# Performance work log

Hardware: AMD Instinct MI355X
Metric: run time of the kernel (lower is better)

Reference implementation:

```python
import jax, jax.numpy as jnp
import numpy as np

N_EMBD = 1024
N_HEAD = 16
HEAD_DIM = N_EMBD // N_HEAD
B, T = 2, 2048


def setup_inputs() -> dict:
    key = jax.random.key(0)
    ks = jax.random.split(key, 12)
    s = 0.02
    inp = {
        "x": jax.random.normal(ks[0], (B, T, N_EMBD), dtype=jnp.float32),
        "ln1_g": jnp.ones((N_EMBD,), jnp.float32),
        "ln1_b": jnp.zeros((N_EMBD,), jnp.float32),
        "ln2_g": jnp.ones((N_EMBD,), jnp.float32),
        "ln2_b": jnp.zeros((N_EMBD,), jnp.float32),
        "W_qkv": jax.random.normal(ks[1], (N_EMBD, 3 * N_EMBD), jnp.float32) * s,
        "b_qkv": jnp.zeros((3 * N_EMBD,), jnp.float32),
        "W_o": jax.random.normal(ks[2], (N_EMBD, N_EMBD), jnp.float32) * s,
        "b_o": jnp.zeros((N_EMBD,), jnp.float32),
        "W_fc": jax.random.normal(ks[3], (N_EMBD, 4 * N_EMBD), jnp.float32) * s,
        "b_fc": jnp.zeros((4 * N_EMBD,), jnp.float32),
        "W_proj": jax.random.normal(ks[4], (4 * N_EMBD, N_EMBD), jnp.float32) * s,
        "b_proj": jnp.zeros((N_EMBD,), jnp.float32),
    }
    return inp


def _layernorm(x, g, b, eps=1e-5):
    mu = jnp.mean(x, axis=-1, keepdims=True)
    var = jnp.var(x, axis=-1, keepdims=True)
    return (x - mu) * jax.lax.rsqrt(var + eps) * g + b


def _block(x, ln1_g, ln1_b, ln2_g, ln2_b, W_qkv, b_qkv, W_o, b_o, W_fc, b_fc, W_proj, b_proj):
    # --- attention sub-block (pre-LN) ---
    h = _layernorm(x, ln1_g, ln1_b)
    qkv = h @ W_qkv + b_qkv                     # [B,T,3E]
    q, k, v = jnp.split(qkv, 3, axis=-1)
    def split_heads(t):
        return t.reshape(B, T, N_HEAD, HEAD_DIM).transpose(0, 2, 1, 3)  # [B,H,T,D]
    q, k, v = split_heads(q), split_heads(k), split_heads(v)
    scores = jnp.einsum("bhqd,bhkd->bhqk", q, k) / (HEAD_DIM ** 0.5)
    causal = jnp.tril(jnp.ones((T, T), dtype=bool))
    scores = jnp.where(causal, scores, jnp.float32(-jnp.inf))
    probs = jax.nn.softmax(scores, axis=-1)
    attn = jnp.einsum("bhqk,bhkd->bhqd", probs, v)        # [B,H,T,D]
    attn = attn.transpose(0, 2, 1, 3).reshape(B, T, N_EMBD)
    x = x + attn @ W_o + b_o
    # --- MLP sub-block (pre-LN) ---
    h = _layernorm(x, ln2_g, ln2_b)
    h = jax.nn.gelu(h @ W_fc + b_fc, approximate=False)
    x = x + h @ W_proj + b_proj
    return x


def reference(x, ln1_g, ln1_b, ln2_g, ln2_b, W_qkv, b_qkv, W_o, b_o, W_fc, b_fc, W_proj, b_proj):
    return _block(x, ln1_g, ln1_b, ln2_g, ln2_b, W_qkv, b_qkv, W_o, b_o, W_fc, b_fc, W_proj, b_proj)
```

## Files before the change

### kernel.cpp

```cpp
#include <hip/hip_runtime.h>
#include <hip/hip_bf16.h>


#define TT 2048
#define EE 1024
#define NH 16
#define HD 64

#define AS1 __attribute__((address_space(1)))
#define AS3 __attribute__((address_space(3)))

using bf16x8 = __bf16 __attribute__((ext_vector_type(8)));
using bf16x4 = __bf16 __attribute__((ext_vector_type(4)));
using f32x4  = float __attribute__((ext_vector_type(4)));

template<int N> __device__ __forceinline__ void vm_wait() {
    if constexpr (N == 0)      asm volatile("s_waitcnt vmcnt(0)" ::: "memory");
    else if constexpr (N == 2) asm volatile("s_waitcnt vmcnt(2)" ::: "memory");
    else if constexpr (N == 3) asm volatile("s_waitcnt vmcnt(3)" ::: "memory");
    else if constexpr (N == 4) asm volatile("s_waitcnt vmcnt(4)" ::: "memory");
    else if constexpr (N == 6) asm volatile("s_waitcnt vmcnt(6)" ::: "memory");
    else                       asm volatile("s_waitcnt vmcnt(8)" ::: "memory");
}

__device__ __forceinline__ float gelu_fast(float v) {
    float z  = v * 0.70710678118f;
    float az = fabsf(z);
    float t  = __builtin_amdgcn_rcpf(__builtin_fmaf(0.3275911f, az, 1.0f));
    float p  = t * __builtin_fmaf(t,
                   __builtin_fmaf(t,
                     __builtin_fmaf(t,
                       __builtin_fmaf(t, 1.061405429f, -1.453152027f),
                       1.421413741f),
                     -0.284496736f),
                   0.254829592f);
    float e  = __expf(-az * az);
    float er = copysignf(1.0f - p * e, z);
    return 0.5f * v * (1.0f + er);
}

__global__ __launch_bounds__(256) void convt_kernel(const float* __restrict__ W,
                                                    __bf16* __restrict__ WT,
                                                    int K, int N) {
    __shared__ __bf16 t[32][33];
    int n0 = blockIdx.x * 32, k0 = blockIdx.y * 32;
    int tid = threadIdx.x;
    int r = tid >> 3, c4 = (tid & 7) * 4;
    float4 v = *(const float4*)(W + (size_t)(k0 + r) * N + n0 + c4);
    t[r][c4 + 0] = (__bf16)v.x; t[r][c4 + 1] = (__bf16)v.y;
    t[r][c4 + 2] = (__bf16)v.z; t[r][c4 + 3] = (__bf16)v.w;
    __syncthreads();
    bf16x4 o;
    o[0] = t[c4 + 0][r]; o[1] = t[c4 + 1][r];
    o[2] = t[c4 + 2][r]; o[3] = t[c4 + 3][r];
    *(bf16x4*)(WT + (size_t)(n0 + r) * K + k0 + c4) = o;
}

__global__ __launch_bounds__(256) void ln_kernel(const float* __restrict__ x,
                                                 const float* __restrict__ g,
                                                 const float* __restrict__ bta,
                                                 __bf16* __restrict__ out) {
    int row = blockIdx.x;
    int tid = threadIdx.x;
    const float4 xv = *(const float4*)(x + (size_t)row * EE + tid * 4);
    float s  = xv.x + xv.y + xv.z + xv.w;
    float ss = xv.x*xv.x + xv.y*xv.y + xv.z*xv.z + xv.w*xv.w;
    __shared__ float rs[256], rss[256];
    rs[tid] = s; rss[tid] = ss;
    __syncthreads();
    for (int st = 128; st > 0; st >>= 1) {
        if (tid < st) { rs[tid] += rs[tid+st]; rss[tid] += rss[tid+st]; }
        __syncthreads();
    }
    float mean = rs[0] * (1.0f / EE);
    float var  = rss[0] * (1.0f / EE) - mean * mean;
    float rstd = rsqrtf(var + 1e-5f);
    const float4 gv = *(const float4*)(g + tid * 4);
    const float4 bv = *(const float4*)(bta + tid * 4);
    bf16x4 ov;
    ov[0] = (__bf16)((xv.x - mean) * rstd * gv.x + bv.x);
    ov[1] = (__bf16)((xv.y - mean) * rstd * gv.y + bv.y);
    ov[2] = (__bf16)((xv.z - mean) * rstd * gv.z + bv.z);
    ov[3] = (__bf16)((xv.w - mean) * rstd * gv.w + bv.w);
    *(bf16x4*)(out + (size_t)row * EE + tid * 4) = ov;
}

template<int TM, int TN, bool GELU, bool RESID, bool QKV, bool ATOMIC, typename CT>
__global__ __launch_bounds__(256) void gemm_bt_kernel(const __bf16* __restrict__ A,
                                                      const __bf16* __restrict__ BT,
                                                      const float* __restrict__ bias,
                                                      const float* resid, CT* C,
                                                      __bf16* vT,
                                                      int M, int N, int K) {
    constexpr int MT = TM / 32;
    constexpr int NT = TN / 32;
    constexpr int LOADS = TM / 64 + TN / 64;
    constexpr int NBUF  = ATOMIC ? 3 : ((LOADS <= 3) ? 4 : 3);
    constexpr int DEPTH = NBUF - 1;
    constexpr int WAITN = (DEPTH - 1) * LOADS;
    __shared__ __align__(16) __bf16 As[NBUF][TM][32];
    __shared__ __align__(16) __bf16 Bs[NBUF][TN][32];
    int tid = threadIdx.x, wave = tid >> 6, lane = tid & 63;
    int quad = lane >> 4, l16 = lane & 15;
    int wm = wave >> 1, wn = wave & 1;
    int m0 = blockIdx.y * TM, n0 = blockIdx.x * TN;

    const int klen = ATOMIC ? (K >> 1) : K;
    const int koff = ATOMIC ? (int)blockIdx.z * klen : 0;

    f32x4 acc[MT][NT] = {};

    int srow = wave * 16 + (lane >> 2);
    int scol = (((lane & 3) ^ ((lane >> 3) & 3)) * 8);
    int xcol = ((quad ^ ((l16 >> 1) & 3)) * 8);

    auto STAGE = [&](int buf, int kt) {
        int kb = koff + (kt << 5);
#pragma unroll
        for (int p = 0; p < TM / 64; p++) {
            const __bf16* g = A + (size_t)(m0 + p * 64 + srow) * K + kb + scol;
            __builtin_amdgcn_global_load_lds((AS1 const void*)g,
                                             (AS3 void*)&As[buf][p * 64 + wave * 16][0],
                                             16, 0, 0);
        }
#pragma unroll
        for (int p = 0; p < TN / 64; p++) {
            const __bf16* g = BT + (size_t)(n0 + p * 64 + srow) * K + kb + scol;
            __builtin_amdgcn_global_load_lds((AS1 const void*)g,
                                             (AS3 void*)&Bs[buf][p * 64 + wave * 16][0],
                                             16, 0, 0);
        }
    };

    auto COMPUTE = [&](int cur) {
        bf16x8 af[MT], bfr[NT];
#pragma unroll
        for (int mt = 0; mt < MT; mt++)
            af[mt] = *(const bf16x8*)(&As[cur][wm * (MT * 16) + mt * 16 + l16][xcol]);
#pragma unroll
        for (int nt = 0; nt < NT; nt++)
            bfr[nt] = *(const bf16x8*)(&Bs[cur][wn * (NT * 16) + nt * 16 + l16][xcol]);
#pragma unroll
        for (int mt = 0; mt < MT; mt++)
#pragma unroll
            for (int nt = 0; nt < NT; nt++)
                acc[mt][nt] = __builtin_amdgcn_mfma_f32_16x16x32_bf16(af[mt], bfr[nt],
                                                                      acc[mt][nt], 0, 0, 0);
    };

    const int nk = klen >> 5;
#pragma unroll
    for (int i = 0; i < DEPTH; ++i) STAGE(i, i);
    vm_wait<WAITN>();
    __builtin_amdgcn_s_barrier();

    int t = 0;
    for (; t + DEPTH < nk; ++t) {
        STAGE((t + DEPTH) % NBUF, t + DEPTH);
        COMPUTE(t % NBUF);
        vm_wait<WAITN>();
        __builtin_amdgcn_s_barrier();
    }
    for (; t < nk; ++t) {
        COMPUTE(t % NBUF);
        if (t + 1 < nk) {
            int rem = nk - 2 - t;
            if (rem >= 1) vm_wait<LOADS>();
            else          vm_wait<0>();
            __builtin_amdgcn_s_barrier();
        }
    }

#pragma unroll
    for (int nt = 0; nt < NT; nt++) {
        int c = n0 + wn * (NT * 16) + nt * 16 + l16;
        float bv = (!ATOMIC || blockIdx.z == 0) ? bias[c] : 0.0f;
#pragma unroll
        for (int mt = 0; mt < MT; mt++) {
#pragma unroll
            for (int r = 0; r < 4; r++) {
                int row = m0 + wm * (MT * 16) + mt * 16 + quad * 4 + r;
                float v = acc[mt][nt][r] + bv;
                if (GELU)  v = gelu_fast(v);
                if (RESID) v += resid[(size_t)row * N + c];
                if (ATOMIC) {
                    atomicAdd((float*)&C[(size_t)row * N + c], v);
                } else if (!QKV) {
                    C[(size_t)row * N + c] = (CT)v;
                } else {
                    if (c < 2 * EE) {
                        ((__bf16*)C)[(size_t)row * (2 * EE) + c] = (__bf16)v;
                    } else {
                        int cv = c - 2 * EE;
                        int bb = row >> 11, tt = row & (TT - 1);
                        vT[((size_t)(bb * NH + (cv >> 6)) * HD + (cv & 63)) * TT + tt] =
                            (__bf16)v;
                    }
                }
            }
        }
    }
}

__global__ __launch_bounds__(64) void flash_attn_kernel(const __bf16* __restrict__ qkv,
                                                        const __bf16* __restrict__ vT,
                                                        __bf16* __restrict__ out) {
    int h = blockIdx.y, b = blockIdx.z;
    int lane = threadIdx.x & 63;
    int quad = lane >> 4, l16 = lane & 15;

    __shared__ __align__(16) __bf16 Ps[16 * 136];

    size_t base = (size_t)b * TT * (2 * EE);
    int qt = (int)gridDim.x - 1 - (int)blockIdx.x;
    int q0 = qt * 16;

    const __bf16* kb2  = qkv + base + EE + h * HD;
    const __bf16* vrow = vT + (size_t)(b * NH + h) * HD * TT + (size_t)l16 * TT + quad * 8;

    const __bf16* qp = qkv + base + (size_t)(q0 + l16) * (2 * EE) + h * HD;
    bf16x8 aq0 = *(const bf16x8*)(qp + quad * 8);
    bf16x8 aq1 = *(const bf16x8*)(qp + 32 + quad * 8);

    f32x4 oacc[4] = {};
    float lsum[4] = {0.f, 0.f, 0.f, 0.f};
    int qg_base = q0 + quad * 4;
    int nIter = (qt >> 3) + 1;

    for (int kt = 0; kt < nIter; ++kt) {
        int k0 = kt * 128;

        bf16x8 bk0[8], bk1[8];
#pragma unroll
        for (int nt = 0; nt < 8; nt++) {
            const __bf16* kp = kb2 + (size_t)(k0 + nt * 16 + l16) * (2 * EE) + quad * 8;
            bk0[nt] = *(const bf16x8*)(kp);
            bk1[nt] = *(const bf16x8*)(kp + 32);
        }

        f32x4 s[8];
#pragma unroll
        for (int nt = 0; nt < 8; nt++) {
            f32x4 z = {};
            z = __builtin_amdgcn_mfma_f32_16x16x32_bf16(aq0, bk0[nt], z, 0, 0, 0);
            s[nt] = __builtin_amdgcn_mfma_f32_16x16x32_bf16(aq1, bk1[nt], z, 0, 0, 0);
        }

        bf16x8 vf[4][4];
#pragma unroll
        for (int dt = 0; dt < 4; dt++)
#pragma unroll
            for (int w = 0; w < 4; w++)
                vf[dt][w] = *(const bf16x8*)(vrow + (size_t)dt * (16 * TT) + k0 + w * 32);

        bool maskt = (kt == nIter - 1);
#pragma unroll
        for (int nt = 0; nt < 8; nt++) {
            int key = k0 + nt * 16 + l16;
            int cb = 2 * nt + (l16 >> 3);
#pragma unroll
            for (int r = 0; r < 4; r++) {
                float p;
                if (maskt && key > qg_base + r) p = 0.0f;
                else p = __expf(fminf(s[nt][r] * 0.125f, 30.0f));
                lsum[r] += p;
                int q = quad * 4 + r;
                int col = (((cb & 8) | ((cb - 2 * q) & 7)) << 3) | (l16 & 7);
                Ps[q * 136 + col] = (__bf16)p;
            }
        }

#pragma unroll
        for (int w = 0; w < 4; w++) {
            int cbr = 4 * w + quad;
            int colr = ((cbr & 8) | ((cbr - 2 * l16) & 7)) << 3;
            bf16x8 ap = *(const bf16x8*)(&Ps[l16 * 136 + colr]);
#pragma unroll
            for (int dt = 0; dt < 4; dt++)
                oacc[dt] = __builtin_amdgcn_mfma_f32_16x16x32_bf16(ap, vf[dt][w],
                                                                   oacc[dt], 0, 0, 0);
        }
    }

#pragma unroll
    for (int off = 1; off < 16; off <<= 1)
#pragma unroll
        for (int r = 0; r < 4; r++) lsum[r] += __shfl_xor(lsum[r], off);
#pragma unroll
    for (int dt = 0; dt < 4; dt++) {
#pragma unroll
        for (int r = 0; r < 4; r++) {
            int qg = qg_base + r;
            out[((size_t)b * TT + qg) * EE + h * HD + dt * 16 + l16] =
                (__bf16)(oacc[dt][r] / lsum[r]);
        }
    }
}

extern "C" void kernel_launch(void* const* d_in, const int* in_sizes, int n_in,
                              void* d_out, int out_size, void* d_ws, size_t ws_size,
                              hipStream_t stream) {
    const float* x     = (const float*)d_in[0];
    const float* ln1g  = (const float*)d_in[1];
    const float* ln1b  = (const float*)d_in[2];
    const float* ln2g  = (const float*)d_in[3];
    const float* ln2b  = (const float*)d_in[4];
    const float* Wqkv  = (const float*)d_in[5];
    const float* bqkv  = (const float*)d_in[6];
    const float* Wo    = (const float*)d_in[7];
    const float* bo    = (const float*)d_in[8];
    const float* Wfc   = (const float*)d_in[9];
    const float* bfc   = (const float*)d_in[10];
    const float* Wproj = (const float*)d_in[11];
    const float* bproj = (const float*)d_in[12];
    float* out = (float*)d_out;

    const int M = 2 * TT;

    __bf16* ws = (__bf16*)d_ws;
    __bf16* regQ   = ws;
    __bf16* regS   = ws + 16777216;
    __bf16* WfcT   = ws + 20971520;
    __bf16* qkv    = regQ;
    __bf16* vT     = regQ + 8388608;
    __bf16* WqkvT  = regQ + 12582912;
    __bf16* WoT    = regQ + 15728640;
    __bf16* ff     = regQ;
    __bf16* h1 = regS, *atn = regS, *h2 = regS;
    __bf16* WprojT = regS;
    float*  x1 = out;

    convt_kernel<<<dim3(3 * EE / 32, EE / 32), 256, 0, stream>>>(Wqkv, WqkvT, EE, 3 * EE);
    convt_kernel<<<dim3(EE / 32, EE / 32), 256, 0, stream>>>(Wo, WoT, EE, EE);
    convt_kernel<<<dim3(4 * EE / 32, EE / 32), 256, 0, stream>>>(Wfc, WfcT, EE, 4 * EE);

    ln_kernel<<<M, 256, 0, stream>>>(x, ln1g, ln1b, h1);
    gemm_bt_kernel<128, 128, false, false, true, false, __bf16>
        <<<dim3(3 * EE / 128, M / 128), 256, 0, stream>>>(
        h1, WqkvT, bqkv, nullptr, qkv, vT, M, 3 * EE, EE);
    flash_attn_kernel<<<dim3(TT / 16, NH, 2), 64, 0, stream>>>(qkv, vT, atn);
    gemm_bt_kernel<128, 64, false, true, false, false, float>
        <<<dim3(EE / 64, M / 128), 256, 0, stream>>>(
        atn, WoT, bo, x, x1, nullptr, M, EE, EE);
    ln_kernel<<<M, 256, 0, stream>>>(x1, ln2g, ln2b, h2);
    gemm_bt_kernel<128, 128, true, false, false, false, __bf16>
        <<<dim3(4 * EE / 128, M / 128), 256, 0, stream>>>(
        h2, WfcT, bfc, nullptr, ff, nullptr, M, 4 * EE, EE);
    convt_kernel<<<dim3(EE / 32, 4 * EE / 32), 256, 0, stream>>>(Wproj, WprojT, 4 * EE, EE);
    gemm_bt_kernel<128, 64, false, false, false, true, float>
        <<<dim3(EE / 64, M / 128, 2), 256, 0, stream>>>(
        ff, WprojT, bproj, nullptr, out, nullptr, M, EE, 4 * EE);
}
```

Measured before the change: 507.1 us.

## Share K tiles across two waves via LDS with register prefetch in flash attention

The attention kernel now runs two waves per block, each handling 16 query rows, so a block covers 32 queries. The K tile for each 128-key step is loaded cooperatively into LDS and shared by both waves, halving global K traffic per query. The next K tile is prefetched into registers while the current one is used. This adds two block barriers per iteration and more LDS use. The wave with earlier queries also processes a fully masked extra key tile on the last iteration.

Result: faster. 472.8 us (-6.7%).

```diff
diff --git a/kernel.cpp b/kernel.cpp
--- a/kernel.cpp
+++ b/kernel.cpp
@@ -202,49 +202,49 @@
     }
 }
 
-__global__ __launch_bounds__(64) void flash_attn_kernel(const __bf16* __restrict__ qkv,
-                                                        const __bf16* __restrict__ vT,
-                                                        __bf16* __restrict__ out) {
+__global__ __launch_bounds__(128) void flash_attn_kernel(const __bf16* __restrict__ qkv,
+                                                         const __bf16* __restrict__ vT,
+                                                         __bf16* __restrict__ out) {
     int h = blockIdx.y, b = blockIdx.z;
-    int lane = threadIdx.x & 63;
+    int tid = threadIdx.x, wave = tid >> 6, lane = tid & 63;
     int quad = lane >> 4, l16 = lane & 15;
 
-    __shared__ __align__(16) __bf16 Ps[16 * 136];
+    __shared__ __align__(16) __bf16 Ks[128 * 72];
+    __shared__ __align__(16) __bf16 Ps[2][16 * 136];
 
     size_t base = (size_t)b * TT * (2 * EE);
+
+    int srow = tid >> 3;
+    int scol = (tid & 7) * 8;
+    const __bf16* kbase = qkv + base + EE + h * HD + scol;
+    const __bf16* vrow = vT + (size_t)(b * NH + h) * HD * TT + (size_t)l16 * TT + quad * 8;
+    __bf16* Psw = &Ps[wave][0];
+
     int qt = (int)gridDim.x - 1 - (int)blockIdx.x;
-    int q0 = qt * 16;
-
-    const __bf16* kb2  = qkv + base + EE + h * HD;
-    const __bf16* vrow = vT + (size_t)(b * NH + h) * HD * TT + (size_t)l16 * TT + quad * 8;
-
-    const __bf16* qp = qkv + base + (size_t)(q0 + l16) * (2 * EE) + h * HD;
+    int q0 = qt * 32;
+
+    int qrow = q0 + wave * 16 + l16;
+    const __bf16* qp = qkv + base + (size_t)qrow * (2 * EE) + h * HD;
     bf16x8 aq0 = *(const bf16x8*)(qp + quad * 8);
     bf16x8 aq1 = *(const bf16x8*)(qp + 32 + quad * 8);
 
     f32x4 oacc[4] = {};
     float lsum[4] = {0.f, 0.f, 0.f, 0.f};
-    int qg_base = q0 + quad * 4;
-    int nIter = (qt >> 3) + 1;
+    int qg_base = q0 + wave * 16 + quad * 4;
+
+    int nIter = (qt >> 2) + 1;
+
+    bf16x8 kr[8];
+#pragma unroll
+    for (int p = 0; p < 8; p++)
+        kr[p] = *(const bf16x8*)(kbase + (size_t)(16 * p + srow) * (2 * EE));
 
     for (int kt = 0; kt < nIter; ++kt) {
         int k0 = kt * 128;
-
-        bf16x8 bk0[8], bk1[8];
-#pragma unroll
-        for (int nt = 0; nt < 8; nt++) {
-            const __bf16* kp = kb2 + (size_t)(k0 + nt * 16 + l16) * (2 * EE) + quad * 8;
-            bk0[nt] = *(const bf16x8*)(kp);
-            bk1[nt] = *(const bf16x8*)(kp + 32);
-        }
-
-        f32x4 s[8];
-#pragma unroll
-        for (int nt = 0; nt < 8; nt++) {
-            f32x4 z = {};
-            z = __builtin_amdgcn_mfma_f32_16x16x32_bf16(aq0, bk0[nt], z, 0, 0, 0);
-            s[nt] = __builtin_amdgcn_mfma_f32_16x16x32_bf16(aq1, bk1[nt], z, 0, 0, 0);
-        }
+#pragma unroll
+        for (int p = 0; p < 8; p++)
+            *(bf16x8*)(&Ks[(16 * p + srow) * 72 + scol]) = kr[p];
+        __syncthreads();
 
         bf16x8 vf[4][4];
 #pragma unroll
@@ -252,6 +252,23 @@
 #pragma unroll
             for (int w = 0; w < 4; w++)
                 vf[dt][w] = *(const bf16x8*)(vrow + (size_t)dt * (16 * TT) + k0 + w * 32);
+
+        if (kt < nIter - 1) {
+            int kn = k0 + 128;
+#pragma unroll
+            for (int p = 0; p < 8; p++)
+                kr[p] = *(const bf16x8*)(kbase + (size_t)(kn + 16 * p + srow) * (2 * EE));
+        }
+
+        f32x4 s[8];
+#pragma unroll
+        for (int nt = 0; nt < 8; nt++) {
+            bf16x8 bk0 = *(const bf16x8*)(&Ks[(nt * 16 + l16) * 72 + quad * 8]);
+            bf16x8 bk1 = *(const bf16x8*)(&Ks[(nt * 16 + l16) * 72 + 32 + quad * 8]);
+            f32x4 z = {};
+            z = __builtin_amdgcn_mfma_f32_16x16x32_bf16(aq0, bk0, z, 0, 0, 0);
+            s[nt] = __builtin_amdgcn_mfma_f32_16x16x32_bf16(aq1, bk1, z, 0, 0, 0);
+        }
 
         bool maskt = (kt == nIter - 1);
 #pragma unroll
@@ -266,7 +283,7 @@
                 lsum[r] += p;
                 int q = quad * 4 + r;
                 int col = (((cb & 8) | ((cb - 2 * q) & 7)) << 3) | (l16 & 7);
-                Ps[q * 136 + col] = (__bf16)p;
+                Psw[q * 136 + col] = (__bf16)p;
             }
         }
 
@@ -274,12 +291,13 @@
         for (int w = 0; w < 4; w++) {
             int cbr = 4 * w + quad;
             int colr = ((cbr & 8) | ((cbr - 2 * l16) & 7)) << 3;
-            bf16x8 ap = *(const bf16x8*)(&Ps[l16 * 136 + colr]);
+            bf16x8 ap = *(const bf16x8*)(&Psw[l16 * 136 + colr]);
 #pragma unroll
             for (int dt = 0; dt < 4; dt++)
                 oacc[dt] = __builtin_amdgcn_mfma_f32_16x16x32_bf16(ap, vf[dt][w],
                                                                    oacc[dt], 0, 0, 0);
         }
+        __syncthreads();
     }
 
 #pragma unroll
@@ -338,7 +356,7 @@
     gemm_bt_kernel<128, 128, false, false, true, false, __bf16>
         <<<dim3(3 * EE / 128, M / 128), 256, 0, stream>>>(
         h1, WqkvT, bqkv, nullptr, qkv, vT, M, 3 * EE, EE);
-    flash_attn_kernel<<<dim3(TT / 16, NH, 2), 64, 0, stream>>>(qkv, vT, atn);
+    flash_attn_kernel<<<dim3(TT / 32, NH, 2), 128, 0, stream>>>(qkv, vT, atn);
     gemm_bt_kernel<128, 64, false, true, false, false, float>
         <<<dim3(EE / 64, M / 128), 256, 0, stream>>>(
         atn, WoT, bo, x, x1, nullptr, M, EE, EE);
```
